# Kernel tuning notes

Hardware: AMD Instinct MI355X
Metric: run time of the kernel (lower is better)

The kernel has to match this reference:

```python
import jax, jax.numpy as jnp
import numpy as np

N_NODES = 100000
N_EDGES = 1600000
IN_DIM = 128
EMB = 64
HID = 2 * EMB  # 128


def gcn_conv(x, W, b, row, col, norm):
    # PyG GCNConv: h = x @ W, then aggregate norm-weighted messages src->dst, then +bias
    h = x @ W                                   # [N, out]
    msg = norm[:, None] * h[row]                # gather over source nodes [E', out]
    out = jax.ops.segment_sum(msg, col, num_segments=N_NODES)  # scatter to targets
    return out + b


def gcn_norm(edge_index, edge_weight, n_nodes):
    # add self-loops with weight 1, then symmetric normalization D^-1/2 A D^-1/2
    loop = jnp.arange(n_nodes, dtype=edge_index.dtype)
    row = jnp.concatenate([edge_index[0], loop])
    col = jnp.concatenate([edge_index[1], loop])
    ew = jnp.concatenate([edge_weight, jnp.ones((n_nodes,), edge_weight.dtype)])
    deg = jax.ops.segment_sum(ew, col, num_segments=n_nodes)
    dinv = jnp.where(deg > 0, jax.lax.rsqrt(deg), 0.0)
    norm = dinv[row] * ew * dinv[col]
    return row, col, norm


def setup_inputs() -> dict:
    key = jax.random.key(0)
    ks = jax.random.split(key, 10)
    x = jax.random.normal(ks[0], (N_NODES, IN_DIM), dtype=jnp.float32)
    edge_index = jax.random.randint(ks[1], (2, N_EDGES), 0, N_NODES, dtype=jnp.int64)
    edge_weight = jax.random.uniform(ks[2], (N_EDGES,), dtype=jnp.float32)
    s1 = 1.0 / np.sqrt(IN_DIM)
    s2 = 1.0 / np.sqrt(HID)
    W1 = jax.random.uniform(ks[3], (IN_DIM, HID), jnp.float32, -s1, s1)
    b1 = jnp.zeros((HID,), jnp.float32)
    Wmu = jax.random.uniform(ks[4], (HID, EMB), jnp.float32, -s2, s2)
    bmu = jnp.zeros((EMB,), jnp.float32)
    Wlv = jax.random.uniform(ks[5], (HID, EMB), jnp.float32, -s2, s2)
    blv = jnp.zeros((EMB,), jnp.float32)
    return {"x": x, "edge_index": edge_index, "edge_weight": edge_weight,
            "W1": W1, "b1": b1, "Wmu": Wmu, "bmu": bmu, "Wlv": Wlv, "blv": blv}


def reference(x, edge_index, edge_weight, W1, b1, Wmu, bmu, Wlv, blv):
    row, col, norm = gcn_norm(edge_index, edge_weight, N_NODES)
    h = jax.nn.relu(gcn_conv(x, W1, b1, row, col, norm))
    mu = gcn_conv(h, Wmu, bmu, row, col, norm)
    logvar = gcn_conv(h, Wlv, blv, row, col, norm)
    return (mu, logvar)
```

## Files before the change

kernel.cpp:

```cpp
#include <hip/hip_runtime.h>

#define NN 100000
#define NE 1600000
#define DD 128
#define OUT_HALF 6400000
#define CAP 64

#define NB 256
#define NPB 391
#define BCAP 8192
#define BSTRIDE 64
#define CHUNK 6144
#define CPT 24

#define GNM 64
#define XPITCH 140

typedef unsigned int uint_t;
typedef float v4f __attribute__((ext_vector_type(4)));
typedef short v8s __attribute__((ext_vector_type(8)));

__device__ __forceinline__ unsigned short f2bf(float f) {
    uint_t u = __float_as_uint(f);
    u = (u + 0x7fffu + ((u >> 16) & 1u)) >> 16;
    return (unsigned short)u;
}
__device__ __forceinline__ float bf2f(unsigned short h) {
    return __uint_as_float(((uint_t)h) << 16);
}
__device__ __forceinline__ float bf_lo(uint_t u) { return __uint_as_float(u << 16); }
__device__ __forceinline__ float bf_hi(uint_t u) { return __uint_as_float(u & 0xffff0000u); }

#define EW_SCALE 32767.0f
#define EW_INV (1.0f / 32767.0f)


__global__ void k_zero(int* __restrict__ bcnt) {
    int i = blockIdx.x * blockDim.x + threadIdx.x;
    if (i < NB * BSTRIDE) bcnt[i] = 0;
}

__launch_bounds__(256)
__global__ void k_bin(const int* __restrict__ row, const int* __restrict__ col,
                      const float* __restrict__ ew, int* __restrict__ bcnt,
                      uint2* __restrict__ bins) {
    __shared__ uint2 sorted[CHUNK];
    __shared__ int hist[NB];
    __shared__ int lstart[NB];
    __shared__ int offs[NB];
    __shared__ int gbase[NB];
    const int tid = threadIdx.x;
    const int ebase = blockIdx.x * CHUNK;
    const int nloc = (NE - ebase < CHUNK) ? (NE - ebase) : CHUNK;

    hist[tid] = 0;
    __syncthreads();

    for (int k = 0; k < CPT; ++k) {
        int i = ebase + k * 256 + tid;
        if (i < NE) {
            uint_t b = (uint_t)col[i] / NPB;
            atomicAdd(&hist[b], 1);
        }
    }
    __syncthreads();

    int v = hist[tid];
#pragma unroll
    for (int s = 1; s < NB; s <<= 1) {
        int t = (tid >= s) ? hist[tid - s] : 0;
        __syncthreads();
        hist[tid] += t;
        __syncthreads();
    }
    int excl = hist[tid] - v;
    lstart[tid] = excl;
    offs[tid] = excl;
    gbase[tid] = atomicAdd(&bcnt[tid * BSTRIDE], v);
    __syncthreads();

    for (int k = 0; k < CPT; ++k) {
        int i = ebase + k * 256 + tid;
        if (i < NE) {
            uint_t c = (uint_t)col[i];
            uint_t r = (uint_t)row[i];
            uint_t q = (uint_t)__float2int_rn(ew[i] * EW_SCALE);
            uint_t b = c / NPB;
            int pos = atomicAdd(&offs[b], 1);
            sorted[pos] = make_uint2((r << 15) | q, c);
        }
    }
    __syncthreads();

    for (int i = tid; i < nloc; i += 256) {
        uint2 rec = sorted[i];
        uint_t b = rec.y / NPB;
        int dst = gbase[b] + (i - lstart[b]);
        if (dst < BCAP) bins[(size_t)b * BCAP + dst] = rec;
    }
}

__launch_bounds__(512)
__global__ void k_scatter(const int* __restrict__ bcnt, const uint2* __restrict__ bins,
                          int* __restrict__ cnt, uint_t* __restrict__ slots,
                          float* __restrict__ dinv) {
    __shared__ int combo[NPB];
    const int b = blockIdx.x;
    const int tid = threadIdx.x;
    if (tid < NPB) combo[tid] = 0;
    __syncthreads();
    int n = bcnt[b * BSTRIDE];
    n = (n < BCAP) ? n : BCAP;
    const int base = b * NPB;
    const uint2* seg = bins + (size_t)b * BCAP;
    for (int i = tid; i < n; i += 512) {
        uint2 rec = seg[i];
        int lc = (int)rec.y - base;
        uint_t w = rec.x & 0x7fffu;
        uint_t old = (uint_t)atomicAdd(&combo[lc], (int)((1u << 22) | w));
        uint_t pos = old >> 22;
        if (pos < CAP) slots[rec.y * CAP + pos] = rec.x;
    }
    __syncthreads();
    if (tid < NPB) {
        int node = base + tid;
        if (node < NN) {
            uint_t v = (uint_t)combo[tid];
            int c = (int)(v >> 22);
            cnt[node] = (c < CAP) ? c : CAP;
            dinv[node] = rsqrtf(1.0f + (float)(v & 0x3fffffu) * EW_INV);
        }
    }
}


template <bool RELU, bool OUT_BF16>
__launch_bounds__(256)
__global__ void k_gather(const uint_t* __restrict__ src, const int* __restrict__ cnt,
                         const uint_t* __restrict__ slots, const float* __restrict__ dinv,
                         const float* __restrict__ bias, void* __restrict__ dst) {
    int wid = (blockIdx.x * blockDim.x + threadIdx.x) >> 6;
    int lane = threadIdx.x & 63;
    if (wid >= NN) return;
    float di = dinv[wid];
    uint_t u = src[wid * 64 + lane];
    float accx = bf_lo(u);
    float accy = bf_hi(u);
    int end = __builtin_amdgcn_readfirstlane(cnt[wid]);
    const uint_t* seg = slots + wid * CAP;
    for (int jj = 0; jj < end; jj += 16) {
        uint_t rp[16];
#pragma unroll
        for (int q = 0; q < 16; ++q) {
            int idx = (jj + q < end) ? (jj + q) : (end - 1);
            rp[q] = seg[idx];
        }
        uint_t sv[16];
#pragma unroll
        for (int q = 0; q < 16; ++q) {
            sv[q] = src[(rp[q] >> 15) * 64 + lane];
        }
#pragma unroll
        for (int q = 0; q < 16; ++q) {
            float p = (jj + q < end) ? (float)(rp[q] & 0x7fffu) * EW_INV : 0.0f;
            accx = fmaf(p, bf_lo(sv[q]), accx);
            accy = fmaf(p, bf_hi(sv[q]), accy);
        }
    }
    accx *= di;
    accy *= di;
    if (RELU) {
        float2 b = ((const float2*)bias)[lane];
        accx = fmaxf(accx + b.x, 0.0f) * di;
        accy = fmaxf(accy + b.y, 0.0f) * di;
    }
    if (OUT_BF16) {
        ((uint_t*)dst)[wid * 64 + lane] =
            (uint_t)f2bf(accx) | ((uint_t)f2bf(accy) << 16);
    } else {
        ((float2*)dst)[wid * 64 + lane] = make_float2(accx, accy);
    }
}


__global__ void k_wpack1(const float* __restrict__ W, unsigned short* __restrict__ P) {
    int e = blockIdx.x * blockDim.x + threadIdx.x;
    if (e >= 2048) return;
    int ln = e & 15, nt = (e >> 4) & 7, la = (e >> 7) & 3, kt = e >> 9;
    v8s v;
#pragma unroll
    for (int j = 0; j < 8; ++j) {
        int k = kt * 32 + la * 4 + (j & 3) + 16 * (j >> 2);
        v[j] = (short)f2bf(W[k * 128 + nt * 16 + ln]);
    }
    *(v8s*)&P[e * 8] = v;
}

__global__ void k_wpack2(const float* __restrict__ Wmu, const float* __restrict__ Wlv,
                         unsigned short* __restrict__ P) {
    int e = blockIdx.x * blockDim.x + threadIdx.x;
    if (e >= 2048) return;
    int ln = e & 15, nt = (e >> 4) & 7, la = (e >> 7) & 3, kt = e >> 9;
    v8s v;
#pragma unroll
    for (int j = 0; j < 8; ++j) {
        int k = kt * 32 + la * 4 + (j & 3) + 16 * (j >> 2);
        float f = (nt < 4) ? Wmu[k * 64 + nt * 16 + ln]
                           : Wlv[k * 64 + (nt - 4) * 16 + ln];
        v[j] = (short)f2bf(f);
    }
    *(v8s*)&P[e * 8] = v;
}


__launch_bounds__(256)
__global__ void k_gemm_h0(const float* __restrict__ X,
                          const unsigned short* __restrict__ Wpk,
                          const float* __restrict__ dinv,
                          unsigned short* __restrict__ Y) {
    __shared__ float xs[GNM * XPITCH];
    const int tid = threadIdx.x;
    const int node0 = blockIdx.x * GNM;

    {
        const float4* X4 = (const float4*)X;
        for (int i = tid; i < GNM * 32; i += 256) {
            int row = i >> 5, kg = i & 31;
            int ne = node0 + row;
            if (ne >= NN) ne = NN - 1;
            *(float4*)&xs[row * XPITCH + kg * 4] = X4[ne * 32 + kg];
        }
    }
    __syncthreads();

    const int wave = tid >> 6, lane = tid & 63;
    const int la = lane >> 4, ln = lane & 15;
    const float* xrow = &xs[(wave * 16 + ln) * XPITCH];
    const v8s* Wf = (const v8s*)Wpk;

    v4f acc[8];
#pragma unroll
    for (int nt = 0; nt < 8; ++nt) acc[nt] = (v4f){0.f, 0.f, 0.f, 0.f};

    for (int kt = 0; kt < 4; ++kt) {
        float4 xa0 = *(const float4*)&xrow[kt * 32 + la * 4];
        float4 xa1 = *(const float4*)&xrow[kt * 32 + la * 4 + 16];
        float xv[8] = {xa0.x, xa0.y, xa0.z, xa0.w, xa1.x, xa1.y, xa1.z, xa1.w};
        v8s ah, al;
#pragma unroll
        for (int j = 0; j < 8; ++j) {
            unsigned short h = f2bf(xv[j]);
            ah[j] = (short)h;
            al[j] = (short)f2bf(xv[j] - bf2f(h));
        }
        const int wbase = (kt * 4 + la) * 8 * 16;
#pragma unroll
        for (int nt = 0; nt < 8; ++nt) {
            v8s bh = Wf[wbase + nt * 16 + ln];
            acc[nt] = __builtin_amdgcn_mfma_f32_16x16x32_bf16(ah, bh, acc[nt], 0, 0, 0);
            acc[nt] = __builtin_amdgcn_mfma_f32_16x16x32_bf16(al, bh, acc[nt], 0, 0, 0);
        }
    }

#pragma unroll
    for (int r = 0; r < 4; ++r) {
        int node = node0 + wave * 16 + la * 4 + r;
        if (node < NN) {
            float di = dinv[node];
#pragma unroll
            for (int nt = 0; nt < 8; ++nt)
                Y[node * 128 + nt * 16 + ln] = f2bf(acc[nt][r] * di);
        }
    }
}

__launch_bounds__(256)
__global__ void k_gemm_out(const float* __restrict__ G,
                           const unsigned short* __restrict__ Wpk,
                           const float* __restrict__ bmu, const float* __restrict__ blv,
                           float* __restrict__ out) {
    __shared__ float xs[GNM * XPITCH];
    const int tid = threadIdx.x;
    const int node0 = blockIdx.x * GNM;

    {
        const float4* G4 = (const float4*)G;
        for (int i = tid; i < GNM * 32; i += 256) {
            int row = i >> 5, kg = i & 31;
            int ne = node0 + row;
            if (ne >= NN) ne = NN - 1;
            *(float4*)&xs[row * XPITCH + kg * 4] = G4[ne * 32 + kg];
        }
    }
    __syncthreads();

    const int wave = tid >> 6, lane = tid & 63;
    const int la = lane >> 4, ln = lane & 15;
    const float* xrow = &xs[(wave * 16 + ln) * XPITCH];
    const v8s* Wf = (const v8s*)Wpk;

    v4f acc[8];
#pragma unroll
    for (int nt = 0; nt < 8; ++nt) acc[nt] = (v4f){0.f, 0.f, 0.f, 0.f};

    for (int kt = 0; kt < 4; ++kt) {
        float4 xa0 = *(const float4*)&xrow[kt * 32 + la * 4];
        float4 xa1 = *(const float4*)&xrow[kt * 32 + la * 4 + 16];
        float xv[8] = {xa0.x, xa0.y, xa0.z, xa0.w, xa1.x, xa1.y, xa1.z, xa1.w};
        v8s ah, al;
#pragma unroll
        for (int j = 0; j < 8; ++j) {
            unsigned short h = f2bf(xv[j]);
            ah[j] = (short)h;
            al[j] = (short)f2bf(xv[j] - bf2f(h));
        }
        const int wbase = (kt * 4 + la) * 8 * 16;
#pragma unroll
        for (int nt = 0; nt < 8; ++nt) {
            v8s bh = Wf[wbase + nt * 16 + ln];
            acc[nt] = __builtin_amdgcn_mfma_f32_16x16x32_bf16(ah, bh, acc[nt], 0, 0, 0);
            acc[nt] = __builtin_amdgcn_mfma_f32_16x16x32_bf16(al, bh, acc[nt], 0, 0, 0);
        }
    }

    float bb[8];
#pragma unroll
    for (int nt = 0; nt < 8; ++nt)
        bb[nt] = (nt < 4) ? bmu[nt * 16 + ln] : blv[(nt - 4) * 16 + ln];

#pragma unroll
    for (int r = 0; r < 4; ++r) {
        int node = node0 + wave * 16 + la * 4 + r;
        if (node < NN) {
#pragma unroll
            for (int nt = 0; nt < 8; ++nt) {
                float v = acc[nt][r] + bb[nt];
                if (nt < 4)
                    out[node * 64 + nt * 16 + ln] = v;
                else
                    out[OUT_HALF + node * 64 + (nt - 4) * 16 + ln] = v;
            }
        }
    }
}


extern "C" void kernel_launch(void* const* d_in, const int* in_sizes, int n_in,
                              void* d_out, int out_size, void* d_ws, size_t ws_size,
                              hipStream_t stream) {
    const float* x   = (const float*)d_in[0];
    const int*   ei  = (const int*)d_in[1];
    const float* ew  = (const float*)d_in[2];
    const float* W1  = (const float*)d_in[3];
    const float* b1  = (const float*)d_in[4];
    const float* Wmu = (const float*)d_in[5];
    const float* bmu = (const float*)d_in[6];
    const float* Wlv = (const float*)d_in[7];
    const float* blv = (const float*)d_in[8];
    const int* rowi = ei;
    const int* coli = ei + NE;
    float* out = (float*)d_out;

    int*    cnt   = (int*)d_ws;
    float*  dinv  = (float*)(cnt + 100352);
    uint_t* slots = (uint_t*)(dinv + 100352);
    float*  poolA = (float*)(slots + NN * CAP);
    uint_t* y0    = (uint_t*)poolA;
    float*  g     = poolA;
    uint_t* y1    = (uint_t*)(poolA + NN * DD);
    uint2*  bins  = (uint2*)poolA;
    int*    bcnt  = (int*)(poolA + NB * BCAP * 2);
    unsigned short* Wpk1 = (unsigned short*)(poolA + NN * 64);
    unsigned short* Wpk2 = (unsigned short*)(poolA + NN * DD);

    const int B = 256;
    const int GGRID = (NN + GNM - 1) / GNM;
    k_zero<<<(NB * BSTRIDE + B - 1) / B, B, 0, stream>>>(bcnt);
    k_bin<<<(NE + CHUNK - 1) / CHUNK, B, 0, stream>>>(rowi, coli, ew, bcnt, bins);
    k_scatter<<<NB, 512, 0, stream>>>(bcnt, bins, cnt, slots, dinv);
    k_wpack1<<<8, B, 0, stream>>>(W1, Wpk1);
    k_gemm_h0<<<GGRID, B, 0, stream>>>(x, Wpk1, dinv, (unsigned short*)y0);
    k_gather<true, true><<<(NN * 64 + B - 1) / B, B, 0, stream>>>(
        y0, cnt, slots, dinv, b1, y1);
    k_gather<false, false><<<(NN * 64 + B - 1) / B, B, 0, stream>>>(
        y1, cnt, slots, dinv, b1, g);
    k_wpack2<<<8, B, 0, stream>>>(Wmu, Wlv, Wpk2);
    k_gemm_out<<<GGRID, B, 0, stream>>>(g, Wpk2, bmu, blv, out);
}
```

Measured before the change: 324.9 us.

## Pad neighbor slots and split gather so each wave covers two nodes' half-columns

Pads each node's slot list up to a multiple of 16 with zero-weight self records so the gather loop no longer needs per-element bounds checks or clamped indices. The gather kernel is restructured so each wave handles two nodes, each half-wave reading 32 columns (128 bytes), and each node's columns are split across two blocks. The intent is shorter, divergence-free inner loops and more independent row gathers in flight. In exchange the scatter step writes padding for every node, half-waves iterate to the larger of the two counts, and each slot list is read twice, once per column half.

```diff
diff --git a/kernel.cpp b/kernel.cpp
--- a/kernel.cpp
+++ b/kernel.cpp
@@ -99,6 +99,7 @@
         if (dst < BCAP) bins[(size_t)b * BCAP + dst] = rec;
     }
 }
+
 
 __launch_bounds__(512)
 __global__ void k_scatter(const int* __restrict__ bcnt, const uint2* __restrict__ bins,
@@ -127,8 +128,11 @@
         if (node < NN) {
             uint_t v = (uint_t)combo[tid];
             int c = (int)(v >> 22);
-            cnt[node] = (c < CAP) ? c : CAP;
+            c = (c < CAP) ? c : CAP;
+            cnt[node] = (c + 15) & ~15;
             dinv[node] = rsqrtf(1.0f + (float)(v & 0x3fffffu) * EW_INV);
+            uint_t padrec = (uint_t)node << 15;
+            for (int j = c; j < CAP; ++j) slots[node * CAP + j] = padrec;
         }
     }
 }
@@ -139,30 +143,32 @@
 __global__ void k_gather(const uint_t* __restrict__ src, const int* __restrict__ cnt,
                          const uint_t* __restrict__ slots, const float* __restrict__ dinv,
                          const float* __restrict__ bias, void* __restrict__ dst) {
-    int wid = (blockIdx.x * blockDim.x + threadIdx.x) >> 6;
-    int lane = threadIdx.x & 63;
-    if (wid >= NN) return;
-    float di = dinv[wid];
-    uint_t u = src[wid * 64 + lane];
+    const int half = blockIdx.x & 1;
+    const int nb = blockIdx.x >> 1;
+    const int tid = threadIdx.x;
+    const int wave = tid >> 6, lane = tid & 63;
+    const int g = lane >> 5, l = lane & 31;
+    const int node = nb * 8 + wave * 2 + g;
+    const int col = half * 32 + l;
+
+    float di = dinv[node];
+    uint_t u = src[node * 64 + col];
     float accx = bf_lo(u);
     float accy = bf_hi(u);
-    int end = __builtin_amdgcn_readfirstlane(cnt[wid]);
-    const uint_t* seg = slots + wid * CAP;
-    for (int jj = 0; jj < end; jj += 16) {
+    int endg = cnt[node];
+    int endo = __shfl_xor(endg, 32);
+    int endmax = (endg > endo) ? endg : endo;
+    const uint_t* seg = slots + node * CAP;
+    for (int jj = 0; jj < endmax; jj += 16) {
         uint_t rp[16];
 #pragma unroll
+        for (int q = 0; q < 16; ++q) rp[q] = seg[jj + q];
+        uint_t sv[16];
+#pragma unroll
+        for (int q = 0; q < 16; ++q) sv[q] = src[(rp[q] >> 15) * 64 + col];
+#pragma unroll
         for (int q = 0; q < 16; ++q) {
-            int idx = (jj + q < end) ? (jj + q) : (end - 1);
-            rp[q] = seg[idx];
-        }
-        uint_t sv[16];
-#pragma unroll
-        for (int q = 0; q < 16; ++q) {
-            sv[q] = src[(rp[q] >> 15) * 64 + lane];
-        }
-#pragma unroll
-        for (int q = 0; q < 16; ++q) {
-            float p = (jj + q < end) ? (float)(rp[q] & 0x7fffu) * EW_INV : 0.0f;
+            float p = (float)(rp[q] & 0x7fffu) * EW_INV;
             accx = fmaf(p, bf_lo(sv[q]), accx);
             accy = fmaf(p, bf_hi(sv[q]), accy);
         }
@@ -170,15 +176,15 @@
     accx *= di;
     accy *= di;
     if (RELU) {
-        float2 b = ((const float2*)bias)[lane];
+        float2 b = ((const float2*)bias)[col];
         accx = fmaxf(accx + b.x, 0.0f) * di;
         accy = fmaxf(accy + b.y, 0.0f) * di;
     }
     if (OUT_BF16) {
-        ((uint_t*)dst)[wid * 64 + lane] =
+        ((uint_t*)dst)[node * 64 + col] =
             (uint_t)f2bf(accx) | ((uint_t)f2bf(accy) << 16);
     } else {
-        ((float2*)dst)[wid * 64 + lane] = make_float2(accx, accy);
+        ((float2*)dst)[node * 64 + col] = make_float2(accx, accy);
     }
 }
 
@@ -375,14 +381,15 @@
 
     const int B = 256;
     const int GGRID = (NN + GNM - 1) / GNM;
+    const int AGGRID = (NN / 8) * 2;
     k_zero<<<(NB * BSTRIDE + B - 1) / B, B, 0, stream>>>(bcnt);
     k_bin<<<(NE + CHUNK - 1) / CHUNK, B, 0, stream>>>(rowi, coli, ew, bcnt, bins);
     k_scatter<<<NB, 512, 0, stream>>>(bcnt, bins, cnt, slots, dinv);
     k_wpack1<<<8, B, 0, stream>>>(W1, Wpk1);
     k_gemm_h0<<<GGRID, B, 0, stream>>>(x, Wpk1, dinv, (unsigned short*)y0);
-    k_gather<true, true><<<(NN * 64 + B - 1) / B, B, 0, stream>>>(
+    k_gather<true, true><<<AGGRID, B, 0, stream>>>(
         y0, cnt, slots, dinv, b1, y1);
-    k_gather<false, false><<<(NN * 64 + B - 1) / B, B, 0, stream>>>(
+    k_gather<false, false><<<AGGRID, B, 0, stream>>>(
         y1, cnt, slots, dinv, b1, g);
     k_wpack2<<<8, B, 0, stream>>>(Wmu, Wlv, Wpk2);
     k_gemm_out<<<GGRID, B, 0, stream>>>(g, Wpk2, bmu, blv, out);
```

Result: no change. 328.6 us (+1.2%).

## Pad neighbor slots to multiples of 16 and shrink binning chunks

Applied to the files above, without the earlier changes.

The scatter kernel now rounds each node's neighbor count up to a multiple of 16 and fills the extra slots with zero-weight self records. This lets the gather loop drop its per-element bounds clamps and masks. The binning kernel uses smaller chunks (2048 edges per block), which gives more blocks, and keeps the column values in registers so they are not loaded twice. The cost is extra slot writes and padded gathers that fetch rows and then multiply them by zero weight.

```diff
diff --git a/kernel.cpp b/kernel.cpp
--- a/kernel.cpp
+++ b/kernel.cpp
@@ -10,8 +10,8 @@
 #define NPB 391
 #define BCAP 8192
 #define BSTRIDE 64
-#define CHUNK 6144
-#define CPT 24
+#define CHUNK 2048
+#define CPT 8
 
 #define GNM 64
 #define XPITCH 140
@@ -56,12 +56,12 @@
     hist[tid] = 0;
     __syncthreads();
 
+    uint_t cols[CPT];
+#pragma unroll
     for (int k = 0; k < CPT; ++k) {
         int i = ebase + k * 256 + tid;
-        if (i < NE) {
-            uint_t b = (uint_t)col[i] / NPB;
-            atomicAdd(&hist[b], 1);
-        }
+        cols[k] = (i < NE) ? (uint_t)col[i] : 0xffffffffu;
+        if (i < NE) atomicAdd(&hist[cols[k] / NPB], 1);
     }
     __syncthreads();
 
@@ -79,14 +79,14 @@
     gbase[tid] = atomicAdd(&bcnt[tid * BSTRIDE], v);
     __syncthreads();
 
+#pragma unroll
     for (int k = 0; k < CPT; ++k) {
         int i = ebase + k * 256 + tid;
         if (i < NE) {
-            uint_t c = (uint_t)col[i];
+            uint_t c = cols[k];
             uint_t r = (uint_t)row[i];
             uint_t q = (uint_t)__float2int_rn(ew[i] * EW_SCALE);
-            uint_t b = c / NPB;
-            int pos = atomicAdd(&offs[b], 1);
+            int pos = atomicAdd(&offs[c / NPB], 1);
             sorted[pos] = make_uint2((r << 15) | q, c);
         }
     }
@@ -99,6 +99,7 @@
         if (dst < BCAP) bins[(size_t)b * BCAP + dst] = rec;
     }
 }
+
 
 __launch_bounds__(512)
 __global__ void k_scatter(const int* __restrict__ bcnt, const uint2* __restrict__ bins,
@@ -127,8 +128,12 @@
         if (node < NN) {
             uint_t v = (uint_t)combo[tid];
             int c = (int)(v >> 22);
-            cnt[node] = (c < CAP) ? c : CAP;
+            c = (c < CAP) ? c : CAP;
+            int cp = (c + 15) & ~15;
+            cnt[node] = cp;
             dinv[node] = rsqrtf(1.0f + (float)(v & 0x3fffffu) * EW_INV);
+            uint_t padrec = (uint_t)node << 15;
+            for (int j = c; j < cp; ++j) slots[node * CAP + j] = padrec;
         }
     }
 }
@@ -151,18 +156,13 @@
     for (int jj = 0; jj < end; jj += 16) {
         uint_t rp[16];
 #pragma unroll
+        for (int q = 0; q < 16; ++q) rp[q] = seg[jj + q];
+        uint_t sv[16];
+#pragma unroll
+        for (int q = 0; q < 16; ++q) sv[q] = src[(rp[q] >> 15) * 64 + lane];
+#pragma unroll
         for (int q = 0; q < 16; ++q) {
-            int idx = (jj + q < end) ? (jj + q) : (end - 1);
-            rp[q] = seg[idx];
-        }
-        uint_t sv[16];
-#pragma unroll
-        for (int q = 0; q < 16; ++q) {
-            sv[q] = src[(rp[q] >> 15) * 64 + lane];
-        }
-#pragma unroll
-        for (int q = 0; q < 16; ++q) {
-            float p = (jj + q < end) ? (float)(rp[q] & 0x7fffu) * EW_INV : 0.0f;
+            float p = (float)(rp[q] & 0x7fffu) * EW_INV;
             accx = fmaf(p, bf_lo(sv[q]), accx);
             accy = fmaf(p, bf_hi(sv[q]), accy);
         }
```

New measurement: 321.6 us. About the same (-1.0%).
